# Performance work log

Hardware: AMD Instinct MI355X
Metric: run time of the kernel (lower is better)

## Reference

```python
import jax, jax.numpy as jnp
import numpy as np

DIM = 1024
HEADS = 16
HEAD_DIM = DIM // HEADS
HIDDEN = 4 * DIM
EPS = 1e-5


def layer_norm(x, g, b):
    mu = jnp.mean(x, axis=-1, keepdims=True)
    var = jnp.mean(jnp.square(x - mu), axis=-1, keepdims=True)
    return (x - mu) * jax.lax.rsqrt(var + EPS) * g + b


def fast_gelu(x):
    # Ascend fast_gelu == x * sigmoid(1.702 * x)
    return x * jax.nn.sigmoid(1.702 * x)


def setup_inputs() -> dict:
    key = jax.random.key(0)
    ks = jax.random.split(key, 12)
    B, N, C = 16, 577, DIM
    s_in = 1.0 / np.sqrt(DIM)
    s_hid = 1.0 / np.sqrt(HIDDEN)
    return {
        "x": jax.random.normal(ks[0], (B * N, C), jnp.float32),
        "norm1_g": jnp.ones((C,), jnp.float32),
        "norm1_b": jnp.zeros((C,), jnp.float32),
        "Wq": jax.random.normal(ks[1], (C, C), jnp.float32) * s_in,
        "Wk": jax.random.normal(ks[2], (C, C), jnp.float32) * s_in,
        "Wv": jax.random.normal(ks[3], (C, C), jnp.float32) * s_in,
        "Wp": jax.random.normal(ks[4], (C, C), jnp.float32) * s_in,
        "bp": jnp.zeros((C,), jnp.float32),
        "norm2_g": jnp.ones((C,), jnp.float32),
        "norm2_b": jnp.zeros((C,), jnp.float32),
        "W1": jax.random.normal(ks[5], (HIDDEN, C), jnp.float32) * s_in,
        "b1": jnp.zeros((HIDDEN,), jnp.float32),
        "W2": jax.random.normal(ks[6], (C, HIDDEN), jnp.float32) * s_hid,
        "b2": jnp.zeros((C,), jnp.float32),
        "B": B,
        "N": N,
        "C": C,
    }


def reference(x, norm1_g, norm1_b, Wq, Wk, Wv, Wp, bp, norm2_g, norm2_b, W1, b1, W2, b2, B, N, C):
    scale = HEAD_DIM ** -0.5

    h = layer_norm(x, norm1_g, norm1_b)          # [B*N, C]
    # qkv projections (qkv_bias=False), reshape to [B, H, N, D]
    def split_heads(y):
        return y.reshape(B, N, HEADS, HEAD_DIM).transpose(0, 2, 1, 3)

    q = split_heads(h @ Wq.T)
    k = split_heads(h @ Wk.T)
    v = split_heads(h @ Wv.T)

    attn = jnp.einsum('bhqd,bhkd->bhqk', q, k) * scale
    attn = jax.nn.softmax(attn, axis=-1)
    o = jnp.einsum('bhqk,bhkd->bhqd', attn, v)   # [B, H, N, D]
    o = o.transpose(0, 2, 1, 3).reshape(B * N, C)
    y = o @ Wp.T + bp                            # attention output proj

    x = x + y                                    # residual 1 (drop_path=0)
    h2 = layer_norm(x, norm2_g, norm2_b)
    m = fast_gelu(h2 @ W1.T + b1) @ W2.T + b2    # MLP (drop=0)
    return x + m                                 # residual 2
```

## Files before the change

### kernel.cpp

```cpp
#include <hip/hip_runtime.h>

typedef short  short8  __attribute__((ext_vector_type(8)));
typedef float  float4v __attribute__((ext_vector_type(4)));

#define DIM      1024
#define HEADS    16
#define HEAD_DIM 64
#define HIDDEN   4096
#define BATCH    16
#define SEQ      577
#define M_ROWS   (BATCH*SEQ)
#define NPAD2    640
#define QKVLD    3072
#define LOG2E    1.4426950408889634f

static __device__ __forceinline__ unsigned short f2bf(float f) {
  unsigned int u = __float_as_uint(f);
  u += 0x7FFFu + ((u >> 16) & 1u);
  return (unsigned short)(u >> 16);
}
static __device__ __forceinline__ void gload_lds16(const void* g, void* l) {
  __builtin_amdgcn_global_load_lds(
      (const __attribute__((address_space(1))) void*)g,
      (__attribute__((address_space(3))) void*)l, 16, 0, 0);
}
static __device__ __forceinline__ int xcd_chunk(int w, int nwg) {
  int xcd = w & 7, rest = w >> 3;
  int q = nwg >> 3, r = nwg & 7;
  int base = xcd < r ? xcd * (q + 1) : r * (q + 1) + (xcd - r) * q;
  return base + rest;
}

__global__ __launch_bounds__(256) void convert_all_kernel(
    const float* __restrict__ Wq, const float* __restrict__ Wk,
    const float* __restrict__ Wv, const float* __restrict__ Wp,
    const float* __restrict__ W1, const float* __restrict__ W2,
    unsigned short* __restrict__ wqkv, unsigned short* __restrict__ wp,
    unsigned short* __restrict__ w1, unsigned short* __restrict__ w2) {
  const int S = DIM * DIM / 4;
  int i = blockIdx.x * 256 + threadIdx.x;
  const float* src; unsigned short* dst; int rel;
  if (i < 4 * S) {
    if (i < S)        { src = Wq; dst = wqkv;               rel = i; }
    else if (i < 2*S) { src = Wk; dst = wqkv + DIM * DIM;   rel = i - S; }
    else if (i < 3*S) { src = Wv; dst = wqkv + 2*DIM*DIM;   rel = i - 2*S; }
    else              { src = Wp; dst = wp;                 rel = i - 3*S; }
  } else if (i < 8*S) { src = W1; dst = w1;                 rel = i - 4*S; }
  else                { src = W2; dst = w2;                 rel = i - 8*S; }
  float4 v = ((const float4*)src)[rel];
  union { unsigned short s[4]; uint2 u; } p;
  p.s[0] = f2bf(v.x); p.s[1] = f2bf(v.y); p.s[2] = f2bf(v.z); p.s[3] = f2bf(v.w);
  ((uint2*)dst)[rel] = p.u;
}

__global__ __launch_bounds__(256) void ln_kernel(
    const float* __restrict__ x, const float* __restrict__ g,
    const float* __restrict__ b, unsigned short* __restrict__ out) {
  int row = blockIdx.x, tid = threadIdx.x;
  const float* xr = x + (long long)row * DIM;
  float4 v = *(const float4*)(xr + tid * 4);
  float s1 = v.x + v.y + v.z + v.w;
  float s2 = v.x*v.x + v.y*v.y + v.z*v.z + v.w*v.w;
  #pragma unroll
  for (int o = 32; o; o >>= 1) { s1 += __shfl_xor(s1, o); s2 += __shfl_xor(s2, o); }
  __shared__ float a1[4], a2[4];
  int wid = tid >> 6, lane = tid & 63;
  if (lane == 0) { a1[wid] = s1; a2[wid] = s2; }
  __syncthreads();
  s1 = a1[0] + a1[1] + a1[2] + a1[3];
  s2 = a2[0] + a2[1] + a2[2] + a2[3];
  float mean = s1 * (1.f / DIM);
  float var  = s2 * (1.f / DIM) - mean * mean;
  float rstd = rsqrtf(var + 1e-5f);
  float4 gv = *(const float4*)(g + tid * 4);
  float4 bv = *(const float4*)(b + tid * 4);
  union { unsigned short s[4]; uint2 u; } p;
  p.s[0] = f2bf((v.x - mean) * rstd * gv.x + bv.x);
  p.s[1] = f2bf((v.y - mean) * rstd * gv.y + bv.y);
  p.s[2] = f2bf((v.z - mean) * rstd * gv.z + bv.z);
  p.s[3] = f2bf((v.w - mean) * rstd * gv.w + bv.w);
  *(uint2*)(out + (long long)row * DIM + tid * 4) = p.u;
}

__global__ __launch_bounds__(256) void transpose_v_kernel(
    const unsigned short* __restrict__ v, unsigned short* __restrict__ vt) {
  int nt0 = blockIdx.x * 64;
  int bh = blockIdx.y;
  int b = bh >> 4, h = bh & 15;
  __shared__ unsigned short T[64][72];
  int tid = threadIdx.x;
  int r = tid >> 3;
  int c = tid & 7;
  #pragma unroll
  for (int p = 0; p < 2; p++) {
    int row = p * 32 + r;
    int n = nt0 + row;
    uint4 val = (uint4){0u, 0u, 0u, 0u};
    if (n < SEQ)
      val = *(const uint4*)(v + ((long long)(b * SEQ + n)) * QKVLD + h * HEAD_DIM + c * 8);
    *(uint4*)&T[row][c * 8] = val;
  }
  __syncthreads();
  #pragma unroll
  for (int p = 0; p < 2; p++) {
    int d = p * 32 + (tid >> 3);
    union { unsigned short s[8]; uint4 u; } o;
    #pragma unroll
    for (int i = 0; i < 8; i++) o.s[i] = T[c * 8 + i][d];
    *(uint4*)(vt + ((long long)bh * HEAD_DIM + d) * NPAD2 + nt0 + c * 8) = o.u;
  }
}

template <bool MASK>
static __device__ __forceinline__ void attn_tile(
    const unsigned short* Ks, const unsigned short* Vs, unsigned short* Ps,
    const short8 (&af)[2][2], float4v (&oacc)[2][4], float4v (&sumacc)[2],
    int quad, int l16, int wid) {
  const float CE = 0.125f * LOG2E;

  short8 bfr[4][2];
  #pragma unroll
  for (int j = 0; j < 4; j++) {
    int r = j * 16 + l16;
    #pragma unroll
    for (int ks = 0; ks < 2; ks++)
      bfr[j][ks] = *(const short8*)(Ks + r * 64 + ((ks * 4 + quad) ^ (l16 & 7)) * 8);
  }

  float4v sacc[2][4];
  #pragma unroll
  for (int i = 0; i < 2; i++)
    #pragma unroll
    for (int j = 0; j < 4; j++) sacc[i][j] = (float4v){0.f, 0.f, 0.f, 0.f};
  #pragma unroll
  for (int i = 0; i < 2; i++)
    #pragma unroll
    for (int j = 0; j < 4; j++)
      #pragma unroll
      for (int ks = 0; ks < 2; ks++)
        sacc[i][j] = __builtin_amdgcn_mfma_f32_16x16x32_bf16(af[i][ks], bfr[j][ks], sacc[i][j], 0, 0, 0);

  #pragma unroll
  for (int i = 0; i < 2; i++) {
    #pragma unroll
    for (int reg = 0; reg < 4; reg++) {
      int prow = wid * 32 + i * 16 + quad * 4 + reg;
      #pragma unroll
      for (int j = 0; j < 4; j++) {
        float pv;
        if constexpr (MASK) {
          pv = (j == 0 && l16 == 0) ? __builtin_amdgcn_exp2f(sacc[i][j][reg] * CE) : 0.f;
        } else {
          pv = __builtin_amdgcn_exp2f(sacc[i][j][reg] * CE);
        }
        int pcol = j * 16 + l16;
        Ps[prow * 64 + (((pcol >> 3) ^ (prow & 7)) * 8) + (pcol & 7)] = f2bf(pv);
      }
    }
  }

  short8 paf[2][2], vbf[4][2];
  #pragma unroll
  for (int i = 0; i < 2; i++) {
    int r = wid * 32 + i * 16 + l16;
    #pragma unroll
    for (int kk = 0; kk < 2; kk++)
      paf[i][kk] = *(const short8*)(Ps + r * 64 + ((kk * 4 + quad) ^ (l16 & 7)) * 8);
  }
  #pragma unroll
  for (int j = 0; j < 4; j++) {
    int r = j * 16 + l16;
    #pragma unroll
    for (int kk = 0; kk < 2; kk++)
      vbf[j][kk] = *(const short8*)(Vs + r * 64 + ((kk * 4 + quad) ^ (l16 & 7)) * 8);
  }
  const short ov = (short)0x3F80;
  const short8 ones = (short8){ov, ov, ov, ov, ov, ov, ov, ov};
  #pragma unroll
  for (int i = 0; i < 2; i++) {
    #pragma unroll
    for (int kk = 0; kk < 2; kk++) {
      #pragma unroll
      for (int j = 0; j < 4; j++)
        oacc[i][j] = __builtin_amdgcn_mfma_f32_16x16x32_bf16(paf[i][kk], vbf[j][kk], oacc[i][j], 0, 0, 0);
      sumacc[i] = __builtin_amdgcn_mfma_f32_16x16x32_bf16(paf[i][kk], ones, sumacc[i], 0, 0, 0);
    }
  }
}

__global__ __launch_bounds__(256, 3) void flash_attn_kernel(
    const unsigned short* __restrict__ q,
    const unsigned short* __restrict__ k,
    const unsigned short* __restrict__ vt,
    unsigned short* __restrict__ o) {
  int w = blockIdx.y * 5 + blockIdx.x;
  int id = xcd_chunk(w, 5 * 256);
  int qt = id % 5;
  int bh = id / 5;
  int b = bh >> 4, h = bh & 15;
  int q0 = qt * 128;
  int tid = threadIdx.x, lane = tid & 63, wid = tid >> 6;
  int quad = lane >> 4, l16 = lane & 15;
  long long rowbase = (long long)b * SEQ;

  __shared__ __align__(16) unsigned short SM[24576];
  unsigned short* Ps = SM + 16384;

  int sr = wid * 16 + (lane >> 3);
  int scc = (lane & 7) ^ (sr & 7);
  const unsigned short* kbase = k + (rowbase + sr) * QKVLD + h * HEAD_DIM + scc * 8;
  const unsigned short* kbase2 = k + (rowbase + sr + 8) * QKVLD + h * HEAD_DIM + (((lane & 7) ^ ((sr + 8) & 7)) * 8);
  const unsigned short* vbase = vt + ((long long)bh * HEAD_DIM + sr) * NPAD2 + scc * 8;
  const unsigned short* vbase2 = vt + ((long long)bh * HEAD_DIM + sr + 8) * NPAD2 + (((lane & 7) ^ ((sr + 8) & 7)) * 8);

  auto stageKV = [&](int sel, int kt) {
    unsigned short* Ks_ = SM + sel * 8192;
    unsigned short* Vs_ = Ks_ + 4096;
    long long koff = (long long)kt * 64 * QKVLD;
    long long koff2 = koff;
    if (kt == 9) {
      koff  -= (long long)((kt * 64 + sr)     - (SEQ - 1) > 0 ? (kt * 64 + sr)     - (SEQ - 1) : 0) * QKVLD;
      koff2 -= (long long)((kt * 64 + sr + 8) - (SEQ - 1) > 0 ? (kt * 64 + sr + 8) - (SEQ - 1) : 0) * QKVLD;
    }
    gload_lds16(kbase  + koff,  Ks_ + sr * 64 - (lane >> 3) * 64);
    gload_lds16(kbase2 + koff2, Ks_ + (sr + 8) * 64 - (lane >> 3) * 64);
    gload_lds16(vbase  + kt * 64, Vs_ + sr * 64 - (lane >> 3) * 64);
    gload_lds16(vbase2 + kt * 64, Vs_ + (sr + 8) * 64 - (lane >> 3) * 64);
  };

  short8 af[2][2];
  #pragma unroll
  for (int i = 0; i < 2; i++) {
    int gr = q0 + wid * 32 + i * 16 + l16;
    if (gr > SEQ - 1) gr = SEQ - 1;
    const unsigned short* qr = q + (rowbase + gr) * QKVLD + h * HEAD_DIM;
    #pragma unroll
    for (int ks = 0; ks < 2; ks++)
      af[i][ks] = *(const short8*)(qr + (ks * 4 + quad) * 8);
  }

  float4v oacc[2][4];
  float4v sumacc[2];
  #pragma unroll
  for (int i = 0; i < 2; i++) {
    sumacc[i] = (float4v){0.f, 0.f, 0.f, 0.f};
    #pragma unroll
    for (int j = 0; j < 4; j++) oacc[i][j] = (float4v){0.f, 0.f, 0.f, 0.f};
  }

  stageKV(0, 0);

  for (int kt = 0; kt < 10; kt++) {
    int cur = kt & 1;
    if (kt < 9) {
      stageKV(cur ^ 1, kt + 1);
      asm volatile("s_waitcnt vmcnt(4)" ::: "memory");
    } else {
      asm volatile("s_waitcnt vmcnt(0)" ::: "memory");
    }
    __builtin_amdgcn_s_barrier();
    const unsigned short* Ks_ = SM + cur * 8192;
    const unsigned short* Vs_ = Ks_ + 4096;
    if (kt < 9) attn_tile<false>(Ks_, Vs_, Ps, af, oacc, sumacc, quad, l16, wid);
    else        attn_tile<true >(Ks_, Vs_, Ps, af, oacc, sumacc, quad, l16, wid);
    asm volatile("" ::: "memory");
    __builtin_amdgcn_s_barrier();
  }

  #pragma unroll
  for (int i = 0; i < 2; i++) {
    #pragma unroll
    for (int reg = 0; reg < 4; reg++) {
      int grow = q0 + wid * 32 + i * 16 + quad * 4 + reg;
      if (grow >= SEQ) continue;
      float inv = 1.f / sumacc[i][reg];
      #pragma unroll
      for (int j = 0; j < 4; j++) {
        int d = j * 16 + l16;
        o[(rowbase + grow) * DIM + h * HEAD_DIM + d] = f2bf(oacc[i][j][reg] * inv);
      }
    }
  }
}

enum { EPI_BF16 = 0, EPI_BIAS_RES_F32 = 2, EPI_BIAS_GELU_BF16 = 3 };

template <int EPI>
__global__ __launch_bounds__(512, 2) void gemm_nt(
    const unsigned short* __restrict__ A, int lda,
    const unsigned short* __restrict__ B, int ldb,
    void* __restrict__ Cout, int ldc,
    const float* __restrict__ bias, const float* __restrict__ res,
    int M, int N, int K) {
  int mt = gridDim.x, nt = gridDim.y;
  int nwg = mt * nt;
  int id = xcd_chunk(blockIdx.y * mt + blockIdx.x, nwg);
  int band  = id / (8 * nt);
  int rem   = id - band * 8 * nt;
  int mrem  = mt - band * 8;
  int bandh = mrem < 8 ? mrem : 8;
  int lm = rem % bandh;
  int nb = rem / bandh;
  int m0 = (band * 8 + lm) * 256, n0 = nb * 256;

  int tid = threadIdx.x;
  int lane = tid & 63, wid = tid >> 6;
  int wm = wid >> 2, wn = wid & 3;
  int quad = lane >> 4, l16 = lane & 15;

  __shared__ __align__(16) unsigned short SMB[65536];

  float4v acc[8][4];
  #pragma unroll
  for (int i = 0; i < 8; i++)
    #pragma unroll
    for (int j = 0; j < 4; j++) acc[i][j] = (float4v){0.f, 0.f, 0.f, 0.f};

  int srow = wid * 32 + (lane >> 2);
  int sc   = (((lane & 3) ^ ((lane >> 3) & 3))) * 8;
  const unsigned short* pA[2];
  const unsigned short* pB[2];
  #pragma unroll
  for (int ii = 0; ii < 2; ii++) {
    int gr = m0 + srow + ii * 16; if (gr > M - 1) gr = M - 1;
    pA[ii] = A + (long long)gr * lda + sc;
    int gn = n0 + srow + ii * 16; if (gn > N - 1) gn = N - 1;
    pB[ii] = B + (long long)gn * ldb + sc;
  }

  auto stage = [&](int u) {
    unsigned short* As_ = SMB + (u & 3) * 16384;
    unsigned short* Bs_ = As_ + 8192;
    int k0 = u << 5;
    #pragma unroll
    for (int ii = 0; ii < 2; ii++) {
      int rbase = (wid * 32 + ii * 16) * 32;
      gload_lds16(pA[ii] + k0, As_ + rbase);
      gload_lds16(pB[ii] + k0, Bs_ + rbase);
    }
  };

  int rsw = (quad ^ ((l16 >> 1) & 3)) << 3;
  auto compute = [&](int u) {
    const unsigned short* As_ = SMB + (u & 3) * 16384;
    const unsigned short* Bs_ = As_ + 8192;
    short8 a[8], b[4];
    #pragma unroll
    for (int mi = 0; mi < 8; mi++)
      a[mi] = *(const short8*)(As_ + (wm * 128 + mi * 16 + l16) * 32 + rsw);
    #pragma unroll
    for (int ni = 0; ni < 4; ni++)
      b[ni] = *(const short8*)(Bs_ + (wn * 64 + ni * 16 + l16) * 32 + rsw);
    __builtin_amdgcn_s_setprio(1);
    #pragma unroll
    for (int mi = 0; mi < 8; mi++)
      #pragma unroll
      for (int ni = 0; ni < 4; ni++)
        acc[mi][ni] = __builtin_amdgcn_mfma_f32_16x16x32_bf16(a[mi], b[ni], acc[mi][ni], 0, 0, 0);
    __builtin_amdgcn_s_setprio(0);
  };

  int U = K >> 5;
  stage(0); stage(1); stage(2);

  for (int p = 0; p < U - 3; p++) {
    stage(p + 3);
    asm volatile("s_waitcnt vmcnt(12)" ::: "memory");
    __builtin_amdgcn_s_barrier();
    __builtin_amdgcn_sched_barrier(0);
    compute(p);
    __builtin_amdgcn_sched_barrier(0);
    __builtin_amdgcn_s_barrier();
  }
  asm volatile("s_waitcnt vmcnt(8)" ::: "memory");
  __builtin_amdgcn_s_barrier();
  __builtin_amdgcn_sched_barrier(0);
  compute(U - 3);
  __builtin_amdgcn_sched_barrier(0);
  __builtin_amdgcn_s_barrier();
  asm volatile("s_waitcnt vmcnt(4)" ::: "memory");
  __builtin_amdgcn_s_barrier();
  __builtin_amdgcn_sched_barrier(0);
  compute(U - 2);
  __builtin_amdgcn_sched_barrier(0);
  __builtin_amdgcn_s_barrier();
  asm volatile("s_waitcnt vmcnt(0)" ::: "memory");
  __builtin_amdgcn_s_barrier();
  __builtin_amdgcn_sched_barrier(0);
  compute(U - 1);
  __builtin_amdgcn_sched_barrier(0);
  __builtin_amdgcn_s_barrier();

  float* cs = (float*)SMB + wid * (16 * 68);
  int erow = lane >> 2;
  int eq   = lane & 3;

  #pragma unroll
  for (int mi = 0; mi < 8; mi++) {
    #pragma unroll
    for (int ni = 0; ni < 4; ni++)
      #pragma unroll
      for (int r = 0; r < 4; r++)
        cs[(quad * 4 + r) * 68 + ni * 16 + l16] = acc[mi][ni][r];
    int grow = m0 + wm * 128 + mi * 16 + erow;
    bool rowok = grow < M;

    if constexpr (EPI == EPI_BIAS_RES_F32) {
      #pragma unroll
      for (int t = 0; t < 4; t++) {
        int colb = t * 16 + eq * 4;
        int gcol = n0 + wn * 64 + colb;
        if (!rowok) continue;
        float4 vv = *(const float4*)&cs[erow * 68 + colb];
        float4 bb = *(const float4*)&bias[gcol];
        const float4 rr = *(const float4*)&res[(long long)grow * ldc + gcol];
        vv.x += bb.x + rr.x; vv.y += bb.y + rr.y;
        vv.z += bb.z + rr.z; vv.w += bb.w + rr.w;
        *(float4*)((float*)Cout + (long long)grow * ldc + gcol) = vv;
      }
    } else {
      #pragma unroll
      for (int h = 0; h < 2; h++) {
        int colb = h * 32 + eq * 8;
        int gcol = n0 + wn * 64 + colb;
        if (!rowok) continue;
        float4 a0 = *(const float4*)&cs[erow * 68 + colb];
        float4 a1 = *(const float4*)&cs[erow * 68 + colb + 4];
        float vs[8] = {a0.x, a0.y, a0.z, a0.w, a1.x, a1.y, a1.z, a1.w};
        if constexpr (EPI == EPI_BIAS_GELU_BF16) {
          float4 b0 = *(const float4*)&bias[gcol];
          float4 b1 = *(const float4*)&bias[gcol + 4];
          float bs[8] = {b0.x, b0.y, b0.z, b0.w, b1.x, b1.y, b1.z, b1.w};
          #pragma unroll
          for (int e = 0; e < 8; e++) {
            float tt = vs[e] + bs[e];
            float ex = __builtin_amdgcn_exp2f(tt * -2.4554669595930156f);
            vs[e] = tt / (1.f + ex);
          }
        }
        union { unsigned short s[8]; uint4 u; } p;
        #pragma unroll
        for (int e = 0; e < 8; e++) p.s[e] = f2bf(vs[e]);
        *(uint4*)((unsigned short*)Cout + (long long)grow * ldc + gcol) = p.u;
      }
    }
  }
}

extern "C" void kernel_launch(void* const* d_in, const int* in_sizes, int n_in,
                              void* d_out, int out_size, void* d_ws, size_t ws_size,
                              hipStream_t stream) {
  const float* x   = (const float*)d_in[0];
  const float* g1  = (const float*)d_in[1];
  const float* be1 = (const float*)d_in[2];
  const float* Wq  = (const float*)d_in[3];
  const float* Wk  = (const float*)d_in[4];
  const float* Wv  = (const float*)d_in[5];
  const float* Wp  = (const float*)d_in[6];
  const float* bp  = (const float*)d_in[7];
  const float* g2  = (const float*)d_in[8];
  const float* be2 = (const float*)d_in[9];
  const float* W1  = (const float*)d_in[10];
  const float* b1  = (const float*)d_in[11];
  const float* W2  = (const float*)d_in[12];
  const float* b2  = (const float*)d_in[13];
  float* out = (float*)d_out;

  char* ws = (char*)d_ws;
  size_t off = 0;
  auto alloc = [&](size_t bytes) {
    size_t r = off; off += (bytes + 255) & ~(size_t)255; return r;
  };
  unsigned short* wqkv_bf = (unsigned short*)(ws + alloc((size_t)3 * DIM * DIM * 2));
  unsigned short* wp_bf   = (unsigned short*)(ws + alloc((size_t)DIM * DIM * 2));
  unsigned short* w1_bf   = (unsigned short*)(ws + alloc((size_t)HIDDEN * DIM * 2));
  unsigned short* w2_bf   = (unsigned short*)(ws + alloc((size_t)HIDDEN * DIM * 2));
  unsigned short* h_bf    = (unsigned short*)(ws + alloc((size_t)M_ROWS * DIM * 2));
  unsigned short* qkv_bf  = (unsigned short*)(ws + alloc((size_t)M_ROWS * QKVLD * 2));
  unsigned short* vt_bf   = (unsigned short*)(ws + alloc((size_t)256 * HEAD_DIM * NPAD2 * 2));

  unsigned short* o_bf  = h_bf;
  unsigned short* h2_bf = h_bf;
  unsigned short* u_bf  = qkv_bf;
  float*          x1    = out;

  convert_all_kernel<<<12 * (DIM * DIM / 4) / 256, 256, 0, stream>>>(
      Wq, Wk, Wv, Wp, W1, W2, wqkv_bf, wp_bf, w1_bf, w2_bf);

  ln_kernel<<<M_ROWS, 256, 0, stream>>>(x, g1, be1, h_bf);

  gemm_nt<EPI_BF16><<<dim3(37, 12), 512, 0, stream>>>(h_bf, DIM, wqkv_bf, DIM,
      qkv_bf, QKVLD, nullptr, nullptr, M_ROWS, 3 * DIM, DIM);

  transpose_v_kernel<<<dim3(10, 256), 256, 0, stream>>>(qkv_bf + 2 * DIM, vt_bf);

  flash_attn_kernel<<<dim3(5, 256), 256, 0, stream>>>(
      qkv_bf, qkv_bf + DIM, vt_bf, o_bf);

  gemm_nt<EPI_BIAS_RES_F32><<<dim3(37, 4), 512, 0, stream>>>(o_bf, DIM, wp_bf, DIM,
      x1, DIM, bp, x, M_ROWS, DIM, DIM);

  ln_kernel<<<M_ROWS, 256, 0, stream>>>(x1, g2, be2, h2_bf);

  gemm_nt<EPI_BIAS_GELU_BF16><<<dim3(37, 16), 512, 0, stream>>>(h2_bf, DIM, w1_bf, DIM,
      u_bf, HIDDEN, b1, nullptr, M_ROWS, HIDDEN, DIM);

  gemm_nt<EPI_BIAS_RES_F32><<<dim3(37, 4), 512, 0, stream>>>(u_bf, HIDDEN, w2_bf, HIDDEN,
      out, DIM, b2, x1, M_ROWS, DIM, HIDDEN);
}
```

Before: 562.1 us.

## Shrink GEMM tile to 128x256 with 5-stage ring and double-buffered register fragments

The GEMM tile drops from 256x256 to 128x256 and the grid grows from 37 to 73 row blocks. This gives more workgroups to fill the CUs and a smaller tail. The LDS ring goes from 4 to 5 stages. Fragment reads from LDS are double-buffered in registers (aA/bA and aB/bB), so the next stage's ds_reads overlap the current MFMAs. The XCD chunk remapping is removed. In exchange, each tile has lower arithmetic intensity, which means more global traffic per FLOP, and the hand-written waitcnt accounting is fragile.

```diff
diff --git a/kernel.cpp b/kernel.cpp
--- a/kernel.cpp
+++ b/kernel.cpp
@@ -293,102 +293,114 @@
     const float* __restrict__ bias, const float* __restrict__ res,
     int M, int N, int K) {
   int mt = gridDim.x, nt = gridDim.y;
-  int nwg = mt * nt;
-  int id = xcd_chunk(blockIdx.y * mt + blockIdx.x, nwg);
+  int id = blockIdx.y * mt + blockIdx.x;
   int band  = id / (8 * nt);
   int rem   = id - band * 8 * nt;
   int mrem  = mt - band * 8;
   int bandh = mrem < 8 ? mrem : 8;
   int lm = rem % bandh;
   int nb = rem / bandh;
-  int m0 = (band * 8 + lm) * 256, n0 = nb * 256;
+  int m0 = (band * 8 + lm) * 128, n0 = nb * 256;
 
   int tid = threadIdx.x;
   int lane = tid & 63, wid = tid >> 6;
-  int wm = wid >> 2, wn = wid & 3;
+  int wm = wid & 1, wn = wid >> 1;
   int quad = lane >> 4, l16 = lane & 15;
 
-  __shared__ __align__(16) unsigned short SMB[65536];
-
-  float4v acc[8][4];
-  #pragma unroll
-  for (int i = 0; i < 8; i++)
+  __shared__ __align__(16) unsigned short SMB[61440];
+
+  float4v acc[4][4];
+  #pragma unroll
+  for (int i = 0; i < 4; i++)
     #pragma unroll
     for (int j = 0; j < 4; j++) acc[i][j] = (float4v){0.f, 0.f, 0.f, 0.f};
 
-  int srow = wid * 32 + (lane >> 2);
-  int sc   = (((lane & 3) ^ ((lane >> 3) & 3))) * 8;
-  const unsigned short* pA[2];
-  const unsigned short* pB[2];
-  #pragma unroll
-  for (int ii = 0; ii < 2; ii++) {
-    int gr = m0 + srow + ii * 16; if (gr > M - 1) gr = M - 1;
-    pA[ii] = A + (long long)gr * lda + sc;
-    int gn = n0 + srow + ii * 16; if (gn > N - 1) gn = N - 1;
-    pB[ii] = B + (long long)gn * ldb + sc;
-  }
+  int srow_q = lane >> 2;
+  int sc = ((lane & 3) ^ ((lane >> 3) & 3)) * 8;
+  int grA = m0 + wid * 16 + srow_q; if (grA > M - 1) grA = M - 1;
+  int gnB1 = n0 + wid * 32 + srow_q;      if (gnB1 > N - 1) gnB1 = N - 1;
+  int gnB2 = n0 + wid * 32 + 16 + srow_q; if (gnB2 > N - 1) gnB2 = N - 1;
+  const unsigned short* pA  = A + (long long)grA  * lda + sc;
+  const unsigned short* pB1 = B + (long long)gnB1 * ldb + sc;
+  const unsigned short* pB2 = B + (long long)gnB2 * ldb + sc;
 
   auto stage = [&](int u) {
-    unsigned short* As_ = SMB + (u & 3) * 16384;
-    unsigned short* Bs_ = As_ + 8192;
+    unsigned short* base = SMB + (u % 5) * 12288;
     int k0 = u << 5;
-    #pragma unroll
-    for (int ii = 0; ii < 2; ii++) {
-      int rbase = (wid * 32 + ii * 16) * 32;
-      gload_lds16(pA[ii] + k0, As_ + rbase);
-      gload_lds16(pB[ii] + k0, Bs_ + rbase);
-    }
+    gload_lds16(pA  + k0, base + wid * 512);
+    gload_lds16(pB1 + k0, base + 4096 + wid * 1024);
+    gload_lds16(pB2 + k0, base + 4096 + wid * 1024 + 512);
   };
 
   int rsw = (quad ^ ((l16 >> 1) & 3)) << 3;
-  auto compute = [&](int u) {
-    const unsigned short* As_ = SMB + (u & 3) * 16384;
-    const unsigned short* Bs_ = As_ + 8192;
-    short8 a[8], b[4];
-    #pragma unroll
-    for (int mi = 0; mi < 8; mi++)
-      a[mi] = *(const short8*)(As_ + (wm * 128 + mi * 16 + l16) * 32 + rsw);
+  auto lread = [&](short8 (&AF)[4], short8 (&BF)[4], int u) {
+    const unsigned short* base = SMB + (u % 5) * 12288;
+    #pragma unroll
+    for (int mi = 0; mi < 4; mi++)
+      AF[mi] = *(const short8*)(base + (wm * 64 + mi * 16 + l16) * 32 + rsw);
     #pragma unroll
     for (int ni = 0; ni < 4; ni++)
-      b[ni] = *(const short8*)(Bs_ + (wn * 64 + ni * 16 + l16) * 32 + rsw);
+      BF[ni] = *(const short8*)(base + 4096 + (wn * 64 + ni * 16 + l16) * 32 + rsw);
+  };
+  auto mfma_blk = [&](short8 (&AF)[4], short8 (&BF)[4]) {
     __builtin_amdgcn_s_setprio(1);
     #pragma unroll
-    for (int mi = 0; mi < 8; mi++)
+    for (int mi = 0; mi < 4; mi++)
       #pragma unroll
       for (int ni = 0; ni < 4; ni++)
-        acc[mi][ni] = __builtin_amdgcn_mfma_f32_16x16x32_bf16(a[mi], b[ni], acc[mi][ni], 0, 0, 0);
+        acc[mi][ni] = __builtin_amdgcn_mfma_f32_16x16x32_bf16(AF[mi], BF[ni], acc[mi][ni], 0, 0, 0);
     __builtin_amdgcn_s_setprio(0);
   };
 
+  short8 aA[4], bA[4], aB[4], bB[4];
   int U = K >> 5;
-  stage(0); stage(1); stage(2);
-
-  for (int p = 0; p < U - 3; p++) {
-    stage(p + 3);
-    asm volatile("s_waitcnt vmcnt(12)" ::: "memory");
+
+  stage(0); stage(1); stage(2); stage(3);
+  asm volatile("s_waitcnt vmcnt(6)" ::: "memory");
+  __builtin_amdgcn_s_barrier();
+  lread(aA, bA, 0);
+
+  for (int p = 0; p < U - 4; p += 2) {
     __builtin_amdgcn_s_barrier();
+    lread(aB, bB, p + 1);
+    stage(p + 4);
+    asm volatile("s_waitcnt vmcnt(6)" ::: "memory");
+    asm volatile("s_waitcnt lgkmcnt(8)" ::: "memory");
     __builtin_amdgcn_sched_barrier(0);
-    compute(p);
+    mfma_blk(aA, bA);
+    __builtin_amdgcn_s_barrier();
+    __builtin_amdgcn_s_barrier();
+    lread(aA, bA, p + 2);
+    stage(p + 5);
+    asm volatile("s_waitcnt vmcnt(6)" ::: "memory");
+    asm volatile("s_waitcnt lgkmcnt(8)" ::: "memory");
     __builtin_amdgcn_sched_barrier(0);
+    mfma_blk(aB, bB);
     __builtin_amdgcn_s_barrier();
   }
-  asm volatile("s_waitcnt vmcnt(8)" ::: "memory");
-  __builtin_amdgcn_s_barrier();
+  __builtin_amdgcn_s_barrier();
+  lread(aB, bB, U - 3);
+  asm volatile("s_waitcnt vmcnt(3)" ::: "memory");
+  asm volatile("s_waitcnt lgkmcnt(8)" ::: "memory");
   __builtin_amdgcn_sched_barrier(0);
-  compute(U - 3);
+  mfma_blk(aA, bA);
+  __builtin_amdgcn_s_barrier();
+  __builtin_amdgcn_s_barrier();
+  lread(aA, bA, U - 2);
+  asm volatile("s_waitcnt vmcnt(0)" ::: "memory");
+  asm volatile("s_waitcnt lgkmcnt(8)" ::: "memory");
   __builtin_amdgcn_sched_barrier(0);
-  __builtin_amdgcn_s_barrier();
-  asm volatile("s_waitcnt vmcnt(4)" ::: "memory");
-  __builtin_amdgcn_s_barrier();
+  mfma_blk(aB, bB);
+  __builtin_amdgcn_s_barrier();
+  __builtin_amdgcn_s_barrier();
+  lread(aB, bB, U - 1);
+  asm volatile("s_waitcnt lgkmcnt(8)" ::: "memory");
   __builtin_amdgcn_sched_barrier(0);
-  compute(U - 2);
+  mfma_blk(aA, bA);
+  __builtin_amdgcn_s_barrier();
+  asm volatile("s_waitcnt lgkmcnt(0)" ::: "memory");
   __builtin_amdgcn_sched_barrier(0);
-  __builtin_amdgcn_s_barrier();
-  asm volatile("s_waitcnt vmcnt(0)" ::: "memory");
-  __builtin_amdgcn_s_barrier();
-  __builtin_amdgcn_sched_barrier(0);
-  compute(U - 1);
-  __builtin_amdgcn_sched_barrier(0);
+  mfma_blk(aB, bB);
   __builtin_amdgcn_s_barrier();
 
   float* cs = (float*)SMB + wid * (16 * 68);
@@ -396,13 +408,13 @@
   int eq   = lane & 3;
 
   #pragma unroll
-  for (int mi = 0; mi < 8; mi++) {
+  for (int mi = 0; mi < 4; mi++) {
     #pragma unroll
     for (int ni = 0; ni < 4; ni++)
       #pragma unroll
       for (int r = 0; r < 4; r++)
         cs[(quad * 4 + r) * 68 + ni * 16 + l16] = acc[mi][ni][r];
-    int grow = m0 + wm * 128 + mi * 16 + erow;
+    int grow = m0 + wm * 64 + mi * 16 + erow;
     bool rowok = grow < M;
 
     if constexpr (EPI == EPI_BIAS_RES_F32) {
@@ -410,7 +422,7 @@
       for (int t = 0; t < 4; t++) {
         int colb = t * 16 + eq * 4;
         int gcol = n0 + wn * 64 + colb;
-        if (!rowok) continue;
+        if (!rowok || gcol >= N) continue;
         float4 vv = *(const float4*)&cs[erow * 68 + colb];
         float4 bb = *(const float4*)&bias[gcol];
         const float4 rr = *(const float4*)&res[(long long)grow * ldc + gcol];
@@ -423,7 +435,7 @@
       for (int h = 0; h < 2; h++) {
         int colb = h * 32 + eq * 8;
         int gcol = n0 + wn * 64 + colb;
-        if (!rowok) continue;
+        if (!rowok || gcol >= N) continue;
         float4 a0 = *(const float4*)&cs[erow * 68 + colb];
         float4 a1 = *(const float4*)&cs[erow * 68 + colb + 4];
         float vs[8] = {a0.x, a0.y, a0.z, a0.w, a1.x, a1.y, a1.z, a1.w};
@@ -489,7 +501,7 @@
 
   ln_kernel<<<M_ROWS, 256, 0, stream>>>(x, g1, be1, h_bf);
 
-  gemm_nt<EPI_BF16><<<dim3(37, 12), 512, 0, stream>>>(h_bf, DIM, wqkv_bf, DIM,
+  gemm_nt<EPI_BF16><<<dim3(73, 12), 512, 0, stream>>>(h_bf, DIM, wqkv_bf, DIM,
       qkv_bf, QKVLD, nullptr, nullptr, M_ROWS, 3 * DIM, DIM);
 
   transpose_v_kernel<<<dim3(10, 256), 256, 0, stream>>>(qkv_bf + 2 * DIM, vt_bf);
@@ -497,14 +509,14 @@
   flash_attn_kernel<<<dim3(5, 256), 256, 0, stream>>>(
       qkv_bf, qkv_bf + DIM, vt_bf, o_bf);
 
-  gemm_nt<EPI_BIAS_RES_F32><<<dim3(37, 4), 512, 0, stream>>>(o_bf, DIM, wp_bf, DIM,
+  gemm_nt<EPI_BIAS_RES_F32><<<dim3(73, 4), 512, 0, stream>>>(o_bf, DIM, wp_bf, DIM,
       x1, DIM, bp, x, M_ROWS, DIM, DIM);
 
   ln_kernel<<<M_ROWS, 256, 0, stream>>>(x1, g2, be2, h2_bf);
 
-  gemm_nt<EPI_BIAS_GELU_BF16><<<dim3(37, 16), 512, 0, stream>>>(h2_bf, DIM, w1_bf, DIM,
+  gemm_nt<EPI_BIAS_GELU_BF16><<<dim3(73, 16), 512, 0, stream>>>(h2_bf, DIM, w1_bf, DIM,
       u_bf, HIDDEN, b1, nullptr, M_ROWS, HIDDEN, DIM);
 
-  gemm_nt<EPI_BIAS_RES_F32><<<dim3(37, 4), 512, 0, stream>>>(u_bf, HIDDEN, w2_bf, HIDDEN,
+  gemm_nt<EPI_BIAS_RES_F32><<<dim3(73, 4), 512, 0, stream>>>(u_bf, HIDDEN, w2_bf, HIDDEN,
       out, DIM, b2, x1, M_ROWS, DIM, HIDDEN);
 }
```

Result: slower. 581.2 us (+3.4%).
